# Performance work log

Measured on AMD Instinct MI355X. Metric: run time of the kernel, lower is better.

The kernel has to match this reference:

```python
import jax, jax.numpy as jnp
import numpy as np

N_NODES = 8192
N_EDGES = 262144
D_IN = 512
D_OUT = 512


def setup_inputs() -> dict:
    key = jax.random.key(0)
    k1, k2, k3 = jax.random.split(key, 3)
    x = jax.random.normal(k1, (N_NODES, D_IN), dtype=jnp.float32)
    edge_index = jax.random.randint(k2, (2, N_EDGES), 0, N_NODES, dtype=jnp.int64)
    weight = jax.random.normal(k3, (D_IN, D_OUT), dtype=jnp.float32)
    bias = jnp.zeros((D_OUT,), dtype=jnp.float32)
    return {"x": x, "edge_index": edge_index, "weight": weight, "bias": bias}


def reference(x, edge_index, weight, bias):
    # GCN layer with selfloop=True branch of the original module.
    n = x.shape[0]
    # Dense symmetric adjacency via scatter-set, matching adj[ei0,ei1]=1; adj[ei1,ei0]=1
    adj = jnp.zeros((n, n), dtype=x.dtype)
    adj = adj.at[edge_index[0], edge_index[1]].set(1.0)
    adj = adj.at[edge_index[1], edge_index[0]].set(1.0)
    # Add self loops, symmetric degree normalization D^{-1/2} A D^{-1/2}
    adj = adj + jnp.eye(n, dtype=x.dtype)
    deg = jnp.sum(adj, axis=1)
    dinv = 1.0 / jnp.sqrt(deg)
    adj = adj * dinv[:, None] * dinv[None, :]  # == D @ adj @ D (diagonal scaling)
    return adj @ (x @ weight) + bias
```

## Files before the change

### kernel.cpp

```cpp
#include <hip/hip_runtime.h>
#include <hip/hip_bf16.h>


#define ELL_STRIDE 128

typedef __attribute__((ext_vector_type(8))) short bf16x8;
typedef __attribute__((ext_vector_type(4))) float f32x4;

__device__ __forceinline__ unsigned short f2bf(float f) {
  unsigned u = __float_as_uint(f);
  u = (u + 0x7fff + ((u >> 16) & 1)) >> 16;
  return (unsigned short)u;
}
__device__ __forceinline__ float bflo(unsigned u) {
  return __uint_as_float(u << 16);
}
__device__ __forceinline__ float bfhi(unsigned u) {
  return __uint_as_float(u & 0xffff0000u);
}

__global__ __launch_bounds__(256) void build_adj_kernel(
    const int* __restrict__ ei, unsigned* __restrict__ mask,
    int n_edges, int words) {
  int e = blockIdx.x * blockDim.x + threadIdx.x;
  if (e >= n_edges) return;
  int u = ei[e];
  int v = ei[e + n_edges];
  atomicOr(&mask[(size_t)u * words + (v >> 5)], 1u << (v & 31));
  atomicOr(&mask[(size_t)v * words + (u >> 5)], 1u << (u & 31));
}

__global__ __launch_bounds__(256) void build_ell_kernel(
    const unsigned* __restrict__ mask, unsigned short* __restrict__ ell,
    int* __restrict__ deg, float* __restrict__ dinv, int n, int words) {
  int gtid = blockIdx.x * blockDim.x + threadIdx.x;
  int node = gtid >> 6;
  int lane = threadIdx.x & 63;
  if (node >= n) return;
  const unsigned* __restrict__ row = mask + (size_t)node * words;
  unsigned short* __restrict__ out = ell + (size_t)node * ELL_STRIDE;

  int running = 0;
  for (int r = 0; r < words; r += 64) {
    const int w = r + lane;
    unsigned bits = row[w];
    const int cnt = __popc(bits);
    int x = cnt;
#pragma unroll
    for (int d = 1; d < 64; d <<= 1) {
      int y = __shfl_up(x, d, 64);
      if (lane >= d) x += y;
    }
    int pos = running + x - cnt;
    while (bits) {
      const int b = __builtin_ctz(bits);
      bits &= bits - 1;
      if (pos < ELL_STRIDE) out[pos] = (unsigned short)((w << 5) + b);
      ++pos;
    }
    running += __shfl(x, 63, 64);
  }
  if (lane == 0) {
    deg[node] = running < ELL_STRIDE ? running : ELL_STRIDE;
    dinv[node] = rsqrtf((float)running + 1.0f);
  }
}

__global__ __launch_bounds__(256) void cast_bf16_kernel(
    const float* __restrict__ in, unsigned short* __restrict__ out, int n4) {
  int t = blockIdx.x * blockDim.x + threadIdx.x;
  if (t >= n4) return;
  float4 v = ((const float4*)in)[t];
  ushort4 o;
  o.x = f2bf(v.x); o.y = f2bf(v.y); o.z = f2bf(v.z); o.w = f2bf(v.w);
  ((ushort4*)out)[t] = o;
}

__global__ __launch_bounds__(256) void transpose_cast_kernel(
    const float* __restrict__ W, unsigned short* __restrict__ Wt, int K, int N) {
  __shared__ float tile[32][33];
  const int tx = threadIdx.x & 31;
  const int ty = threadIdx.x >> 5;
  const int bx = blockIdx.x, by = blockIdx.y;
#pragma unroll
  for (int r = 0; r < 4; ++r)
    tile[ty + 8 * r][tx] = W[(size_t)(by * 32 + ty + 8 * r) * N + bx * 32 + tx];
  __syncthreads();
#pragma unroll
  for (int r = 0; r < 4; ++r)
    Wt[(size_t)(bx * 32 + ty + 8 * r) * K + by * 32 + tx] =
        f2bf(tile[tx][ty + 8 * r]);
}

__global__ __launch_bounds__(256) void gemm_mfma_kernel(
    const unsigned short* __restrict__ xb,
    const unsigned short* __restrict__ Wt,
    const float* __restrict__ dinv,
    unsigned short* __restrict__ Hs,
    int M, int N, int K) {
  __shared__ unsigned short As[512 * 8];
  __shared__ unsigned short Bs[512 * 8];

  const int tid = threadIdx.x;
  const int wave = tid >> 6;
  const int lane = tid & 63;
  const int q = lane >> 4;
  const int c = lane & 15;
  const int m0 = blockIdx.y * 128;
  const int n0 = blockIdx.x * 128;
  const int wr = wave >> 1, wc = wave & 1;

  f32x4 acc[4][4] = {};

  for (int k0 = 0; k0 < K; k0 += 32) {
#pragma unroll
    for (int t = 0; t < 2; ++t) {
      const int sbase = wave * 128 + t * 64;
      const int s = sbase + lane;
      const int kc = s >> 7, row = s & 127;
      const unsigned short* g = xb + (size_t)(m0 + row) * K + k0 + kc * 8;
      __builtin_amdgcn_global_load_lds(
          (const __attribute__((address_space(1))) void*)g,
          (__attribute__((address_space(3))) void*)(As + sbase * 8), 16, 0, 0);
    }
#pragma unroll
    for (int t = 0; t < 2; ++t) {
      const int sbase = wave * 128 + t * 64;
      const int s = sbase + lane;
      const int n = s >> 2, kc = s & 3;
      const unsigned short* g = Wt + (size_t)(n0 + n) * K + k0 + kc * 8;
      __builtin_amdgcn_global_load_lds(
          (const __attribute__((address_space(1))) void*)g,
          (__attribute__((address_space(3))) void*)(Bs + sbase * 8), 16, 0, 0);
    }
    __syncthreads();

    bf16x8 a[4], b[4];
#pragma unroll
    for (int tm = 0; tm < 4; ++tm) {
      const int row = wr * 64 + tm * 16 + c;
      a[tm] = *(const bf16x8*)(As + (q * 128 + row) * 8);
    }
#pragma unroll
    for (int tn = 0; tn < 4; ++tn) {
      const int n = wc * 64 + tn * 16 + c;
      b[tn] = *(const bf16x8*)(Bs + (n * 4 + q) * 8);
    }
#pragma unroll
    for (int tm = 0; tm < 4; ++tm)
#pragma unroll
      for (int tn = 0; tn < 4; ++tn)
        acc[tm][tn] = __builtin_amdgcn_mfma_f32_16x16x32_bf16(
            a[tm], b[tn], acc[tm][tn], 0, 0, 0);
    __syncthreads();
  }

#pragma unroll
  for (int tm = 0; tm < 4; ++tm) {
#pragma unroll
    for (int r = 0; r < 4; ++r) {
      const int grow = m0 + wr * 64 + tm * 16 + q * 4 + r;
      const float di = dinv[grow];
#pragma unroll
      for (int tn = 0; tn < 4; ++tn) {
        const int gcol = n0 + wc * 64 + tn * 16 + c;
        Hs[(size_t)grow * N + gcol] = f2bf(di * acc[tm][tn][r]);
      }
    }
  }
}

__global__ __launch_bounds__(256) void spmm_kernel(
    const unsigned short* __restrict__ ell, const int* __restrict__ deg,
    const unsigned short* __restrict__ Hs, const float* __restrict__ dinv,
    const float* __restrict__ bias, float* __restrict__ out, int n, int D) {
  const int i = blockIdx.x;
  const int tid = threadIdx.x;
  const int wave = tid >> 6, lane = tid & 63;
  __shared__ unsigned short jl[ELL_STRIDE];
  __shared__ float red[4][512];

  if (tid < ELL_STRIDE) jl[tid] = ell[(size_t)i * ELL_STRIDE + tid];
  __syncthreads();
  const int dcount = deg[i];

  const unsigned short* __restrict__ hb = Hs + lane * 8;
  float acc[8] = {0.f, 0.f, 0.f, 0.f, 0.f, 0.f, 0.f, 0.f};
#pragma unroll 4
  for (int k = wave; k < dcount; k += 4) {
    const int j = jl[k];
    const uint4 h = *(const uint4*)(hb + (size_t)j * D);
    acc[0] += bflo(h.x); acc[1] += bfhi(h.x);
    acc[2] += bflo(h.y); acc[3] += bfhi(h.y);
    acc[4] += bflo(h.z); acc[5] += bfhi(h.z);
    acc[6] += bflo(h.w); acc[7] += bfhi(h.w);
  }
  *(float4*)&red[wave][lane * 8]     = make_float4(acc[0], acc[1], acc[2], acc[3]);
  *(float4*)&red[wave][lane * 8 + 4] = make_float4(acc[4], acc[5], acc[6], acc[7]);
  __syncthreads();

  const float di = dinv[i];
  const int c0 = tid * 2;
  float s0 = red[0][c0] + red[1][c0] + red[2][c0] + red[3][c0];
  float s1 = red[0][c0 + 1] + red[1][c0 + 1] + red[2][c0 + 1] + red[3][c0 + 1];
  const unsigned selfw = ((const unsigned*)(Hs + (size_t)i * D))[tid];
  const float2 bb = ((const float2*)bias)[tid];
  float2 o;
  o.x = di * (s0 + bflo(selfw)) + bb.x;
  o.y = di * (s1 + bfhi(selfw)) + bb.y;
  ((float2*)out)[(size_t)i * (D / 2) + tid] = o;
}

extern "C" void kernel_launch(void* const* d_in, const int* in_sizes, int n_in,
                              void* d_out, int out_size, void* d_ws, size_t ws_size,
                              hipStream_t stream) {
  const float* x    = (const float*)d_in[0];
  const int*   ei   = (const int*)d_in[1];
  const float* W    = (const float*)d_in[2];
  const float* bias = (const float*)d_in[3];
  float* out = (float*)d_out;

  const int d_out_dim = in_sizes[3];
  const int d_in_dim  = in_sizes[2] / d_out_dim;
  const int n_nodes   = in_sizes[0] / d_in_dim;
  const int n_edges   = in_sizes[1] / 2;
  const int words     = (n_nodes + 31) / 32;

  char* ws = (char*)d_ws;
  size_t off = 0;
  unsigned* mask = (unsigned*)(ws + off); off += (size_t)n_nodes * words * 4;
  float* dinv    = (float*)(ws + off);    off += (size_t)n_nodes * 4;
  int* deg       = (int*)(ws + off);      off += (size_t)n_nodes * 4;
  unsigned short* ell = (unsigned short*)(ws + off); off += (size_t)n_nodes * ELL_STRIDE * 2;
  unsigned short* xb  = (unsigned short*)(ws + off); off += (size_t)n_nodes * d_in_dim * 2;
  unsigned short* Wt  = (unsigned short*)(ws + off); off += (size_t)d_in_dim * d_out_dim * 2;
  unsigned short* Hs  = (unsigned short*)(ws + off); off += (size_t)n_nodes * d_out_dim * 2;

  hipMemsetAsync(mask, 0, (size_t)n_nodes * words * sizeof(unsigned), stream);

  build_adj_kernel<<<(n_edges + 255) / 256, 256, 0, stream>>>(ei, mask, n_edges, words);

  build_ell_kernel<<<(n_nodes * 64 + 255) / 256, 256, 0, stream>>>(mask, ell, deg, dinv,
                                                                   n_nodes, words);

  const int n4 = n_nodes * d_in_dim / 4;
  cast_bf16_kernel<<<(n4 + 255) / 256, 256, 0, stream>>>(x, xb, n4);

  dim3 tgrid(d_out_dim / 32, d_in_dim / 32);
  transpose_cast_kernel<<<tgrid, 256, 0, stream>>>(W, Wt, d_in_dim, d_out_dim);

  dim3 ggrid(d_out_dim / 128, n_nodes / 128);
  gemm_mfma_kernel<<<ggrid, 256, 0, stream>>>(xb, Wt, dinv, Hs,
                                              n_nodes, d_out_dim, d_in_dim);

  spmm_kernel<<<n_nodes, 256, 0, stream>>>(ell, deg, Hs, dinv, bias, out,
                                           n_nodes, d_out_dim);
}
```

Measured before the change: 166.3 us.

## Assign one SpMM row per wave and drop cross-wave LDS reduction

Restructures the SpMM so each wavefront handles a whole row instead of four waves splitting one row's neighbor list. This removes the shared-memory reduction and both block barriers, and folds the self-loop term and bias into vectorized per-lane writes. In exchange each wave iterates over the full neighbor list serially, relying on more resident waves and deeper unrolling to hide gather latency.

```diff
diff --git a/kernel.cpp b/kernel.cpp
--- a/kernel.cpp
+++ b/kernel.cpp
@@ -174,41 +174,42 @@
     const unsigned short* __restrict__ ell, const int* __restrict__ deg,
     const unsigned short* __restrict__ Hs, const float* __restrict__ dinv,
     const float* __restrict__ bias, float* __restrict__ out, int n, int D) {
-  const int i = blockIdx.x;
-  const int tid = threadIdx.x;
-  const int wave = tid >> 6, lane = tid & 63;
-  __shared__ unsigned short jl[ELL_STRIDE];
-  __shared__ float red[4][512];
-
-  if (tid < ELL_STRIDE) jl[tid] = ell[(size_t)i * ELL_STRIDE + tid];
-  __syncthreads();
-  const int dcount = deg[i];
+  __shared__ unsigned short jl[4][ELL_STRIDE];
+  const int wave = threadIdx.x >> 6, lane = threadIdx.x & 63;
+  const int i = blockIdx.x * 4 + wave;
+
+  jl[wave][lane] = ell[(size_t)i * ELL_STRIDE + lane];
+  jl[wave][64 + lane] = ell[(size_t)i * ELL_STRIDE + 64 + lane];
+  const int d = deg[i];
 
   const unsigned short* __restrict__ hb = Hs + lane * 8;
   float acc[8] = {0.f, 0.f, 0.f, 0.f, 0.f, 0.f, 0.f, 0.f};
-#pragma unroll 4
-  for (int k = wave; k < dcount; k += 4) {
-    const int j = jl[k];
+#pragma unroll 8
+  for (int k = 0; k < d; ++k) {
+    const int j = jl[wave][k];
     const uint4 h = *(const uint4*)(hb + (size_t)j * D);
     acc[0] += bflo(h.x); acc[1] += bfhi(h.x);
     acc[2] += bflo(h.y); acc[3] += bfhi(h.y);
     acc[4] += bflo(h.z); acc[5] += bfhi(h.z);
     acc[6] += bflo(h.w); acc[7] += bfhi(h.w);
   }
-  *(float4*)&red[wave][lane * 8]     = make_float4(acc[0], acc[1], acc[2], acc[3]);
-  *(float4*)&red[wave][lane * 8 + 4] = make_float4(acc[4], acc[5], acc[6], acc[7]);
-  __syncthreads();
+
+  const uint4 hs = *(const uint4*)(hb + (size_t)i * D);
+  acc[0] += bflo(hs.x); acc[1] += bfhi(hs.x);
+  acc[2] += bflo(hs.y); acc[3] += bfhi(hs.y);
+  acc[4] += bflo(hs.z); acc[5] += bfhi(hs.z);
+  acc[6] += bflo(hs.w); acc[7] += bfhi(hs.w);
 
   const float di = dinv[i];
-  const int c0 = tid * 2;
-  float s0 = red[0][c0] + red[1][c0] + red[2][c0] + red[3][c0];
-  float s1 = red[0][c0 + 1] + red[1][c0 + 1] + red[2][c0 + 1] + red[3][c0 + 1];
-  const unsigned selfw = ((const unsigned*)(Hs + (size_t)i * D))[tid];
-  const float2 bb = ((const float2*)bias)[tid];
-  float2 o;
-  o.x = di * (s0 + bflo(selfw)) + bb.x;
-  o.y = di * (s1 + bfhi(selfw)) + bb.y;
-  ((float2*)out)[(size_t)i * (D / 2) + tid] = o;
+  const float4 b0 = *(const float4*)(bias + lane * 8);
+  const float4 b1 = *(const float4*)(bias + lane * 8 + 4);
+  float4 o0, o1;
+  o0.x = di * acc[0] + b0.x; o0.y = di * acc[1] + b0.y;
+  o0.z = di * acc[2] + b0.z; o0.w = di * acc[3] + b0.w;
+  o1.x = di * acc[4] + b1.x; o1.y = di * acc[5] + b1.y;
+  o1.z = di * acc[6] + b1.z; o1.w = di * acc[7] + b1.w;
+  *(float4*)(out + (size_t)i * D + lane * 8) = o0;
+  *(float4*)(out + (size_t)i * D + lane * 8 + 4) = o1;
 }
 
 extern "C" void kernel_launch(void* const* d_in, const int* in_sizes, int n_in,
@@ -253,6 +254,6 @@
   gemm_mfma_kernel<<<ggrid, 256, 0, stream>>>(xb, Wt, dinv, Hs,
                                               n_nodes, d_out_dim, d_in_dim);
 
-  spmm_kernel<<<n_nodes, 256, 0, stream>>>(ell, deg, Hs, dinv, bias, out,
-                                           n_nodes, d_out_dim);
-}
+  spmm_kernel<<<n_nodes / 4, 256, 0, stream>>>(ell, deg, Hs, dinv, bias, out,
+                                               n_nodes, d_out_dim);
+}
```

Result: no change. 163.4 us (-1.8%).
